# Kernel optimization log

Measured on AMD Instinct MI355X. Metric: run time of the kernel, lower is better.

## Reference

```python
import jax, jax.numpy as jnp
import numpy as np

L = 2          # num encoder layers
D = 256        # node_dim / d_model
H = 4          # nhead
FF = 4 * D     # dim_feedforward
GEO = 8        # geo feature dim (bi ++ bj)
HID = 512      # relation MLP hidden
C = 56         # num_rel_classes
N = 384        # number of nodes


def layer_norm(x, g, b, eps=1e-5):
    mu = jnp.mean(x, axis=-1, keepdims=True)
    var = jnp.mean((x - mu) ** 2, axis=-1, keepdims=True)
    return (x - mu) * jax.lax.rsqrt(var + eps) * g + b


def encoder_layer(x, wi, bi, wo, bo, w1, b1, w2, b2, g1, be1, g2, be2):
    # Post-norm torch TransformerEncoderLayer (norm_first=False, relu)
    n = x.shape[0]
    dh = D // H
    qkv = x @ wi + bi                                  # [n, 3D]
    q, k, v = jnp.split(qkv, 3, axis=-1)
    q = q.reshape(n, H, dh)
    k = k.reshape(n, H, dh)
    v = v.reshape(n, H, dh)
    scores = jnp.einsum('nhd,mhd->hnm', q, k) * (dh ** -0.5)
    attn = jax.nn.softmax(scores, axis=-1)
    o = jnp.einsum('hnm,mhd->nhd', attn, v).reshape(n, D) @ wo + bo
    x = layer_norm(x + o, g1, be1)
    f = jax.nn.relu(x @ w1 + b1) @ w2 + b2
    x = layer_norm(x + f, g2, be2)
    return x


def setup_inputs() -> dict:
    key = jax.random.key(0)
    ks = jax.random.split(key, 16)
    s = 0.02
    f32 = jnp.float32
    return {
        'node_feats': jax.random.normal(ks[0], (N, D), f32),
        'boxes_norm': jax.random.uniform(ks[1], (N, 4), dtype=f32),
        'attn_w_in': jax.random.normal(ks[2], (L, D, 3 * D), f32) * s,
        'attn_b_in': jnp.zeros((L, 3 * D), f32),
        'attn_w_out': jax.random.normal(ks[3], (L, D, D), f32) * s,
        'attn_b_out': jnp.zeros((L, D), f32),
        'ffn_w1': jax.random.normal(ks[4], (L, D, FF), f32) * s,
        'ffn_b1': jnp.zeros((L, FF), f32),
        'ffn_w2': jax.random.normal(ks[5], (L, FF, D), f32) * s,
        'ffn_b2': jnp.zeros((L, D), f32),
        'ln1_g': jnp.ones((L, D), f32),
        'ln1_b': jnp.zeros((L, D), f32),
        'ln2_g': jnp.ones((L, D), f32),
        'ln2_b': jnp.zeros((L, D), f32),
        'mlp_w1': jax.random.normal(ks[6], (2 * D + GEO, HID), f32) * s,
        'mlp_b1': jnp.zeros((HID,), f32),
        'mlp_w2': jax.random.normal(ks[7], (HID, C), f32) * s,
        'mlp_b2': jnp.zeros((C,), f32),
    }


def reference(node_feats, boxes_norm, attn_w_in, attn_b_in, attn_w_out,
              attn_b_out, ffn_w1, ffn_b1, ffn_w2, ffn_b2, ln1_g, ln1_b,
              ln2_g, ln2_b, mlp_w1, mlp_b1, mlp_w2, mlp_b2):
    x = node_feats
    for l in range(L):
        x = encoder_layer(x, attn_w_in[l], attn_b_in[l], attn_w_out[l],
                          attn_b_out[l], ffn_w1[l], ffn_b1[l], ffn_w2[l],
                          ffn_b2[l], ln1_g[l], ln1_b[l], ln2_g[l], ln2_b[l])
    n = node_feats.shape[0]
    # all ordered pairs (i, j), i != j, in row-major order matching the loop
    i_full = np.repeat(np.arange(n), n)
    j_full = np.tile(np.arange(n), n)
    keep = i_full != j_full
    idx_i = jnp.asarray(i_full[keep])
    idx_j = jnp.asarray(j_full[keep])
    rel_in = jnp.concatenate(
        [x[idx_i], x[idx_j], boxes_norm[idx_i], boxes_norm[idx_j]], axis=1)
    rel_logits = jax.nn.relu(rel_in @ mlp_w1 + mlp_b1) @ mlp_w2 + mlp_b2
    pair_idx = jnp.stack([idx_i, idx_j], axis=1)
    return (pair_idx, rel_logits)
```

## Files before the change

### kernel.cpp

```cpp
#include <hip/hip_runtime.h>

#define NN 384
#define DM 256
#define NH 4
#define FF 1024
#define HIDN 512
#define NCLS 56
#define NPAIR (NN*(NN-1))

typedef __attribute__((ext_vector_type(8))) short short8v;
typedef __attribute__((ext_vector_type(4))) float f32x4;
typedef __attribute__((ext_vector_type(16))) float f32x16;
typedef __attribute__((ext_vector_type(8))) unsigned short ushort8;
typedef __attribute__((ext_vector_type(4))) unsigned int uint4v;

static __device__ __forceinline__ unsigned short f2bf(float f) {
  unsigned u = __float_as_uint(f);
  unsigned r = u + 0x7fff + ((u >> 16) & 1);
  return (unsigned short)(r >> 16);
}
static __device__ __forceinline__ float bf2f(unsigned short v) {
  return __uint_as_float(((unsigned)v) << 16);
}
static __device__ __forceinline__ unsigned cvt_pk_bf16(float lo, float hi) {
  unsigned r;
  asm("v_cvt_pk_bf16_f32 %0, %1, %2" : "=v"(r) : "v"(lo), "v"(hi));
  return r;
}
#define MLROW(reg, half) (((reg) & 3) + 8 * ((reg) >> 2) + 4 * (half))

__global__ __launch_bounds__(256)
void pack_all(const float* __restrict__ wi, const float* __restrict__ wo,
              const float* __restrict__ w1, const float* __restrict__ w2,
              const float* __restrict__ mw1, const float* __restrict__ mw2,
              unsigned short* __restrict__ wi_f, unsigned short* __restrict__ wo_f,
              unsigned short* __restrict__ w1_f, unsigned short* __restrict__ w2_f,
              unsigned short* __restrict__ mw1_f, unsigned short* __restrict__ mw2_f) {
  int y = blockIdx.y, z = blockIdx.z;
  int t = blockIdx.x * 256 + threadIdx.x;
  const float* src; unsigned short* dst; int K, N; long sS, sD;
  switch (y) {
    case 0: src = wi;  dst = wi_f;  K = 256;  N = 768;  sS = 256L*768;  sD = 196608; break;
    case 1: src = wo;  dst = wo_f;  K = 256;  N = 256;  sS = 256L*256;  sD = 65536;  break;
    case 2: src = w1;  dst = w1_f;  K = 256;  N = 1024; sS = 256L*1024; sD = 262144; break;
    case 3: src = w2;  dst = w2_f;  K = 1024; N = 256;  sS = 1024L*256; sD = 262144; break;
    case 4: src = mw1; dst = mw1_f; K = 256;  N = 512;  sS = 256L*512;  sD = 131072; break;
    default: {
      if (z || t >= 4096) return;
      int l = t & 63, nt = (t >> 6) & 1, ks = t >> 7;
      int kb = ks * 16 + ((l >> 5) * 8), n = nt * 32 + (l & 31);
      #pragma unroll
      for (int r = 0; r < 8; ++r) {
        float v = (n < NCLS) ? mw2[(size_t)(kb + r) * NCLS + n] : 0.f;
        mw2_f[(size_t)t * 8 + r] = f2bf(v);
      }
      return;
    }
  }
  int Nt = N >> 5;
  int total = (K >> 4) * Nt * 64;
  if (t >= total) return;
  src += z * sS; dst += z * sD;
  int l = t & 63;
  int rem = t >> 6;
  int nt = rem % Nt, ks = rem / Nt;
  int kb = ks * 16 + ((l >> 5) * 8), n = nt * 32 + (l & 31);
  #pragma unroll
  for (int r = 0; r < 8; ++r)
    dst[(size_t)t * 8 + r] = f2bf(src[(size_t)(kb + r) * N + n]);
}

__global__ __launch_bounds__(256)
void x_init(const float* __restrict__ node, float* __restrict__ xbuf,
            unsigned short* __restrict__ xbf) {
  int i = blockIdx.x * 256 + threadIdx.x;
  float v = node[i];
  xbuf[i] = v;
  xbf[i] = f2bf(v);
}

__global__ __launch_bounds__(128)
void qkv_mfma(const unsigned short* __restrict__ xbf, const unsigned short* __restrict__ wif,
              const float* __restrict__ bi, unsigned short* __restrict__ qk,
              unsigned short* __restrict__ vt) {
  int id = blockIdx.x * 2 + (threadIdx.x >> 6);
  int lane = threadIdx.x & 63;
  int mt = id % 12, nt = id / 12;
  int col = lane & 31, half = lane >> 5;
  const unsigned short* asrc = xbf + (size_t)(mt * 32 + col) * 256 + half * 8;
  const unsigned short* bsrc = wif + ((size_t)nt * 64 + lane) * 8;
  f32x16 acc = {};
  #pragma unroll
  for (int ks = 0; ks < 16; ++ks) {
    short8v a = *reinterpret_cast<const short8v*>(asrc + ks * 16);
    short8v b = *reinterpret_cast<const short8v*>(bsrc + (size_t)ks * 24 * 512);
    acc = __builtin_amdgcn_mfma_f32_32x32x16_bf16(a, b, acc, 0, 0, 0);
  }
  int n = nt * 32 + col;
  float bb = bi[n];
  #pragma unroll
  for (int reg = 0; reg < 16; ++reg) {
    int row = mt * 32 + MLROW(reg, half);
    float v = acc[reg] + bb;
    if (n < 512) qk[(size_t)row * 512 + n] = f2bf(v);
    else         vt[(size_t)(n - 512) * 384 + row] = f2bf(v);
  }
}

__global__ __launch_bounds__(256)
void fused_attn(const unsigned short* __restrict__ qk, const unsigned short* __restrict__ vt,
                unsigned short* __restrict__ attno) {
  __shared__ float S[32][385];
  __shared__ unsigned short P[32][392];
  int n0 = blockIdx.x * 32;
  int h = blockIdx.y;
  int wave = threadIdx.x >> 6, lane = threadIdx.x & 63;
  int col = lane & 31, half = lane >> 5;
  {
    const unsigned short* asrc = qk + (size_t)(n0 + col) * 512 + h * 64 + half * 8;
    #pragma unroll
    for (int jj = 0; jj < 3; ++jj) {
      int ntk = wave * 3 + jj;
      const unsigned short* bsrc = qk + (size_t)(ntk * 32 + col) * 512 + 256 + h * 64 + half * 8;
      f32x16 acc = {};
      #pragma unroll
      for (int ks = 0; ks < 4; ++ks) {
        short8v a = *reinterpret_cast<const short8v*>(asrc + ks * 16);
        short8v b = *reinterpret_cast<const short8v*>(bsrc + ks * 16);
        acc = __builtin_amdgcn_mfma_f32_32x32x16_bf16(a, b, acc, 0, 0, 0);
      }
      #pragma unroll
      for (int reg = 0; reg < 16; ++reg)
        S[MLROW(reg, half)][ntk * 32 + col] = acc[reg] * 0.125f;
    }
  }
  __syncthreads();
  {
    int row = threadIdx.x >> 3, q = threadIdx.x & 7;
    float mx = -1e30f;
    #pragma unroll 8
    for (int c = 0; c < 48; ++c) mx = fmaxf(mx, S[row][q * 48 + c]);
    mx = fmaxf(mx, __shfl_xor(mx, 1));
    mx = fmaxf(mx, __shfl_xor(mx, 2));
    mx = fmaxf(mx, __shfl_xor(mx, 4));
    float sum = 0.f;
    #pragma unroll 8
    for (int c = 0; c < 48; ++c) {
      float e = __expf(S[row][q * 48 + c] - mx);
      S[row][q * 48 + c] = e;
      sum += e;
    }
    sum += __shfl_xor(sum, 1);
    sum += __shfl_xor(sum, 2);
    sum += __shfl_xor(sum, 4);
    float inv = 1.0f / sum;
    #pragma unroll 8
    for (int c = 0; c < 48; ++c)
      P[row][q * 48 + c] = f2bf(S[row][q * 48 + c] * inv);
  }
  __syncthreads();
  if (wave < 2) {
    int ntd = wave;
    const unsigned short* bsrc = vt + (size_t)(h * 64 + ntd * 32 + col) * 384 + half * 8;
    f32x16 acc = {};
    #pragma unroll
    for (int ks = 0; ks < 24; ++ks) {
      short8v a = *reinterpret_cast<const short8v*>(&P[col][ks * 16 + half * 8]);
      short8v b = *reinterpret_cast<const short8v*>(bsrc + ks * 16);
      acc = __builtin_amdgcn_mfma_f32_32x32x16_bf16(a, b, acc, 0, 0, 0);
    }
    #pragma unroll
    for (int reg = 0; reg < 16; ++reg)
      attno[(size_t)(n0 + MLROW(reg, half)) * 256 + h * 64 + ntd * 32 + col] =
          f2bf(acc[reg]);
  }
}

__global__ __launch_bounds__(256)
void add_ln(float* __restrict__ x, unsigned short* __restrict__ xbf,
            const float* __restrict__ r,
            const float* __restrict__ g, const float* __restrict__ b) {
  int i = blockIdx.x, t = threadIdx.x;
  float v = x[(size_t)i * DM + t] + r[(size_t)i * DM + t];
  __shared__ float red[256];
  red[t] = v; __syncthreads();
  for (int s = 128; s > 0; s >>= 1) { if (t < s) red[t] += red[t + s]; __syncthreads(); }
  float mu = red[0] * (1.0f / DM); __syncthreads();
  float dv = v - mu;
  red[t] = dv * dv; __syncthreads();
  for (int s = 128; s > 0; s >>= 1) { if (t < s) red[t] += red[t + s]; __syncthreads(); }
  float var = red[0] * (1.0f / DM);
  float inv = rsqrtf(var + 1e-5f);
  float o = dv * inv * g[t] + b[t];
  x[(size_t)i * DM + t] = o;
  xbf[(size_t)i * DM + t] = f2bf(o);
}

template<int OUT_BF16, int RELU, int NKS, int NT>
__global__ void mfma_gemm(const unsigned short* __restrict__ A, int lda, long sA,
               const unsigned short* __restrict__ Bfrag, long sB,
               const float* __restrict__ bias,
               float* __restrict__ Cf, unsigned short* __restrict__ Cb,
               int ldc, long sC, int Mt) {
  int id = blockIdx.x * (blockDim.x >> 6) + (threadIdx.x >> 6);
  if (id >= Mt * NT) return;
  int lane = threadIdx.x & 63;
  int mt = id % Mt, nt = id / Mt;
  int z = blockIdx.z;
  int col = lane & 31, half = lane >> 5;
  const unsigned short* asrc = A + z * sA + (size_t)(mt * 32 + col) * lda + half * 8;
  const unsigned short* bsrc = Bfrag + z * sB + ((size_t)nt * 64 + lane) * 8;
  f32x16 acc = {};
  #pragma unroll
  for (int ks = 0; ks < NKS; ++ks) {
    short8v a = *reinterpret_cast<const short8v*>(asrc + ks * 16);
    short8v b = *reinterpret_cast<const short8v*>(bsrc + (size_t)ks * NT * 512);
    acc = __builtin_amdgcn_mfma_f32_32x32x16_bf16(a, b, acc, 0, 0, 0);
  }
  int n = nt * 32 + col;
  float bb = bias ? bias[n] : 0.f;
  #pragma unroll
  for (int reg = 0; reg < 16; ++reg) {
    int row = mt * 32 + MLROW(reg, half);
    float v = acc[reg] + bb;
    if (RELU) v = fmaxf(v, 0.f);
    if (OUT_BF16) Cb[z * sC + (size_t)row * ldc + n] = f2bf(v);
    else          Cf[z * sC + (size_t)row * ldc + n] = v;
  }
}

__global__ __launch_bounds__(128)
void uv_gemm(const unsigned short* __restrict__ xbf, const unsigned short* __restrict__ mw1f,
             const float* __restrict__ mw1, const float* __restrict__ b1,
             const float* __restrict__ boxes,
             float* __restrict__ U, unsigned short* __restrict__ Vbf) {
  int id = blockIdx.x * 2 + (threadIdx.x >> 6);
  int lane = threadIdx.x & 63;
  int z = blockIdx.z;
  int mt = id % 12, nt = id / 12;
  int col = lane & 31, half = lane >> 5;
  const unsigned short* asrc = xbf + (size_t)(mt * 32 + col) * 256 + half * 8;
  const unsigned short* bsrc = mw1f + (size_t)z * 131072 + ((size_t)nt * 64 + lane) * 8;
  f32x16 acc = {};
  #pragma unroll
  for (int ks = 0; ks < 16; ++ks) {
    short8v a = *reinterpret_cast<const short8v*>(asrc + ks * 16);
    short8v b = *reinterpret_cast<const short8v*>(bsrc + (size_t)ks * 16 * 512);
    acc = __builtin_amdgcn_mfma_f32_32x32x16_bf16(a, b, acc, 0, 0, 0);
  }
  int n = nt * 32 + col;
  float w0 = mw1[(size_t)(512 + z * 4 + 0) * HIDN + n];
  float w1r = mw1[(size_t)(512 + z * 4 + 1) * HIDN + n];
  float w2r = mw1[(size_t)(512 + z * 4 + 2) * HIDN + n];
  float w3 = mw1[(size_t)(512 + z * 4 + 3) * HIDN + n];
  float bb = (z == 0) ? b1[n] : 0.f;
  #pragma unroll
  for (int reg = 0; reg < 16; ++reg) {
    int row = mt * 32 + MLROW(reg, half);
    const float* bx = boxes + row * 4;
    float v = acc[reg] + bb + bx[0] * w0 + bx[1] * w1r + bx[2] * w2r + bx[3] * w3;
    if (z == 0) U[(size_t)row * HIDN + n] = v;
    else        Vbf[(size_t)row * HIDN + n] = f2bf(v);
  }
}

__global__ __launch_bounds__(256)
void pair_idx_kernel(float* __restrict__ out) {
  int p = blockIdx.x * 256 + threadIdx.x;
  if (p >= NPAIR) return;
  int i = p / (NN - 1);
  int r = p - i * (NN - 1);
  int j = r + (r >= i ? 1 : 0);
  out[2 * p + 0] = (float)i;
  out[2 * p + 1] = (float)j;
}

__global__ __launch_bounds__(512, 2)
void pair_mfma(const float* __restrict__ U, const unsigned short* __restrict__ Vbf,
               const unsigned short* __restrict__ w2frag,
               const float* __restrict__ b2, float* __restrict__ out) {
  __shared__ unsigned short w2l[32768];
  #pragma unroll
  for (int p = 0; p < 8; ++p) {
    int off = p * 4096 + threadIdx.x * 8;
    *reinterpret_cast<uint4v*>(&w2l[off]) =
        *reinterpret_cast<const uint4v*>(w2frag + off);
  }
  __syncthreads();

  int wave = threadIdx.x >> 6, lane = threadIdx.x & 63;
  int task = blockIdx.x * 8 + wave;
  int ip = task / 12, jt = task % 12;
  int i0 = ip * 2;
  int col = lane & 31, half = lane >> 5;
  int j_row = jt * 32 + col;

  const unsigned short* vsrc = Vbf + (size_t)j_row * HIDN + half * 8;
  const float* u0 = U + (size_t)i0 * HIDN + half * 8;
  const float* u1 = u0 + HIDN;
  const unsigned short* bsrc = w2l + (size_t)lane * 8;

  f32x16 acc00 = {}, acc01 = {}, acc10 = {}, acc11 = {};
  #pragma unroll
  for (int ks = 0; ks < 32; ++ks) {
    ushort8 v8 = *reinterpret_cast<const ushort8*>(vsrc + ks * 16);
    short8v b0 = *reinterpret_cast<const short8v*>(bsrc + (size_t)(ks * 2 + 0) * 512);
    short8v b1v = *reinterpret_cast<const short8v*>(bsrc + (size_t)(ks * 2 + 1) * 512);
    float4 ua0 = *reinterpret_cast<const float4*>(u0 + ks * 16);
    float4 ub0 = *reinterpret_cast<const float4*>(u0 + ks * 16 + 4);
    float4 ua1 = *reinterpret_cast<const float4*>(u1 + ks * 16);
    float4 ub1 = *reinterpret_cast<const float4*>(u1 + ks * 16 + 4);
    float v0 = bf2f(v8[0]), v1 = bf2f(v8[1]), v2 = bf2f(v8[2]), v3 = bf2f(v8[3]);
    float v4 = bf2f(v8[4]), v5 = bf2f(v8[5]), v6 = bf2f(v8[6]), v7 = bf2f(v8[7]);
    uint4v pk0;
    pk0[0] = cvt_pk_bf16(fmaxf(v0 + ua0.x, 0.f), fmaxf(v1 + ua0.y, 0.f));
    pk0[1] = cvt_pk_bf16(fmaxf(v2 + ua0.z, 0.f), fmaxf(v3 + ua0.w, 0.f));
    pk0[2] = cvt_pk_bf16(fmaxf(v4 + ub0.x, 0.f), fmaxf(v5 + ub0.y, 0.f));
    pk0[3] = cvt_pk_bf16(fmaxf(v6 + ub0.z, 0.f), fmaxf(v7 + ub0.w, 0.f));
    short8v a0 = *reinterpret_cast<short8v*>(&pk0);
    acc00 = __builtin_amdgcn_mfma_f32_32x32x16_bf16(a0, b0, acc00, 0, 0, 0);
    acc01 = __builtin_amdgcn_mfma_f32_32x32x16_bf16(a0, b1v, acc01, 0, 0, 0);
    uint4v pk1;
    pk1[0] = cvt_pk_bf16(fmaxf(v0 + ua1.x, 0.f), fmaxf(v1 + ua1.y, 0.f));
    pk1[1] = cvt_pk_bf16(fmaxf(v2 + ua1.z, 0.f), fmaxf(v3 + ua1.w, 0.f));
    pk1[2] = cvt_pk_bf16(fmaxf(v4 + ub1.x, 0.f), fmaxf(v5 + ub1.y, 0.f));
    pk1[3] = cvt_pk_bf16(fmaxf(v6 + ub1.z, 0.f), fmaxf(v7 + ub1.w, 0.f));
    short8v a1 = *reinterpret_cast<short8v*>(&pk1);
    acc10 = __builtin_amdgcn_mfma_f32_32x32x16_bf16(a1, b0, acc10, 0, 0, 0);
    acc11 = __builtin_amdgcn_mfma_f32_32x32x16_bf16(a1, b1v, acc11, 0, 0, 0);
  }

  float b2v0 = b2[col];
  float b2v1 = (32 + col < NCLS) ? b2[32 + col] : 0.f;
  float* lg = out + 2 * (size_t)NPAIR;
  int i1 = i0 + 1;
  #pragma unroll
  for (int reg = 0; reg < 16; ++reg) {
    int j = jt * 32 + MLROW(reg, half);
    if (j != i0) {
      int p = i0 * (NN - 1) + (j > i0 ? j - 1 : j);
      float* row = lg + (size_t)p * NCLS;
      row[col] = acc00[reg] + b2v0;
      if (col < NCLS - 32) row[32 + col] = acc01[reg] + b2v1;
    }
    if (j != i1) {
      int p = i1 * (NN - 1) + (j > i1 ? j - 1 : j);
      float* row = lg + (size_t)p * NCLS;
      row[col] = acc10[reg] + b2v0;
      if (col < NCLS - 32) row[32 + col] = acc11[reg] + b2v1;
    }
  }
}

extern "C" void kernel_launch(void* const* d_in, const int* in_sizes, int n_in,
                              void* d_out, int out_size, void* d_ws, size_t ws_size,
                              hipStream_t stream) {
  const float* node   = (const float*)d_in[0];
  const float* boxes  = (const float*)d_in[1];
  const float* w_in   = (const float*)d_in[2];
  const float* b_in   = (const float*)d_in[3];
  const float* w_out  = (const float*)d_in[4];
  const float* b_out  = (const float*)d_in[5];
  const float* fw1    = (const float*)d_in[6];
  const float* fb1    = (const float*)d_in[7];
  const float* fw2    = (const float*)d_in[8];
  const float* fb2    = (const float*)d_in[9];
  const float* ln1g   = (const float*)d_in[10];
  const float* ln1b   = (const float*)d_in[11];
  const float* ln2g   = (const float*)d_in[12];
  const float* ln2b   = (const float*)d_in[13];
  const float* mw1    = (const float*)d_in[14];
  const float* mb1    = (const float*)d_in[15];
  const float* mw2    = (const float*)d_in[16];
  const float* mb2    = (const float*)d_in[17];
  float* out = (float*)d_out;

  float* ws = (float*)d_ws;
  float* xbuf = ws;
  float* proj = xbuf + 98304;
  float* U    = proj + 98304;
  unsigned short* us = (unsigned short*)(U + 196608);
  unsigned short* x_bf   = us;             us += 98304;
  unsigned short* qk_bf  = us;             us += 196608;
  unsigned short* vt_bf  = us;             us += 98304;
  unsigned short* at_bf  = us;             us += 98304;
  unsigned short* ffh_bf = us;             us += 393216;
  unsigned short* Vbf    = us;             us += 196608;
  unsigned short* wi_f   = us;             us += 393216;
  unsigned short* wo_f   = us;             us += 131072;
  unsigned short* fw1_f  = us;             us += 524288;
  unsigned short* fw2_f  = us;             us += 524288;
  unsigned short* mw1_f  = us;             us += 262144;
  unsigned short* w2_f   = us;             us += 32768;

  pack_all<<<dim3(128, 6, 2), 256, 0, stream>>>(w_in, w_out, fw1, fw2, mw1, mw2,
                                                wi_f, wo_f, fw1_f, fw2_f, mw1_f, w2_f);
  pair_idx_kernel<<<dim3((NPAIR + 255) / 256), 256, 0, stream>>>(out);
  x_init<<<dim3(384), 256, 0, stream>>>(node, xbuf, x_bf);

  for (int l = 0; l < 2; ++l) {
    qkv_mfma<<<dim3(144), 128, 0, stream>>>(x_bf, wi_f + (size_t)l * 196608,
                                            b_in + (size_t)l * 768, qk_bf, vt_bf);
    fused_attn<<<dim3(12, 4), 256, 0, stream>>>(qk_bf, vt_bf, at_bf);
    mfma_gemm<0, 0, 16, 8><<<dim3(48), 128, 0, stream>>>(
        at_bf, 256, 0, wo_f + (size_t)l * 65536, 0, b_out + (size_t)l * 256,
        proj, nullptr, 256, 0, 12);
    add_ln<<<dim3(NN), 256, 0, stream>>>(xbuf, x_bf, proj,
                                         ln1g + (size_t)l * 256, ln1b + (size_t)l * 256);
    mfma_gemm<1, 1, 16, 32><<<dim3(192), 128, 0, stream>>>(
        x_bf, 256, 0, fw1_f + (size_t)l * 262144, 0, fb1 + (size_t)l * 1024,
        nullptr, ffh_bf, 1024, 0, 12);
    mfma_gemm<0, 0, 64, 8><<<dim3(48), 128, 0, stream>>>(
        ffh_bf, 1024, 0, fw2_f + (size_t)l * 262144, 0, fb2 + (size_t)l * 256,
        proj, nullptr, 256, 0, 12);
    add_ln<<<dim3(NN), 256, 0, stream>>>(xbuf, x_bf, proj,
                                         ln2g + (size_t)l * 256, ln2b + (size_t)l * 256);
  }

  uv_gemm<<<dim3(96, 1, 2), 128, 0, stream>>>(x_bf, mw1_f, mw1, mb1, boxes, U, Vbf);
  pair_mfma<<<dim3(288), 512, 0, stream>>>(U, Vbf, w2_f, mb2, out);
}
```

Before: 136.9 us.

## Fuse encoder stages into one persistent kernel with global barriers

Replaces the chain of roughly twenty small kernel launches (weight packing, init, QKV, attention, projections, layernorms, FFN, UV GEMM) with a single persistent 48-block kernel that separates stages with atomic-counter grid barriers. Layernorm is rewritten to use one wave per row with shuffle reductions and single-pass mean and variance. The aim is to remove launch overhead and tail gaps between the many tiny stages. In exchange, only 48 blocks run, so each stage has far less parallelism than its own launch had. The spin barrier also depends on all 48 blocks being resident at once, and the counter is cleared by a memset every call.

```diff
diff --git a/kernel.cpp b/kernel.cpp
--- a/kernel.cpp
+++ b/kernel.cpp
@@ -7,6 +7,7 @@
 #define HIDN 512
 #define NCLS 56
 #define NPAIR (NN*(NN-1))
+#define NBLK 48
 
 typedef __attribute__((ext_vector_type(8))) short short8v;
 typedef __attribute__((ext_vector_type(4))) float f32x4;
@@ -29,187 +30,21 @@
 }
 #define MLROW(reg, half) (((reg) & 3) + 8 * ((reg) >> 2) + 4 * (half))
 
-__global__ __launch_bounds__(256)
-void pack_all(const float* __restrict__ wi, const float* __restrict__ wo,
-              const float* __restrict__ w1, const float* __restrict__ w2,
-              const float* __restrict__ mw1, const float* __restrict__ mw2,
-              unsigned short* __restrict__ wi_f, unsigned short* __restrict__ wo_f,
-              unsigned short* __restrict__ w1_f, unsigned short* __restrict__ w2_f,
-              unsigned short* __restrict__ mw1_f, unsigned short* __restrict__ mw2_f) {
-  int y = blockIdx.y, z = blockIdx.z;
-  int t = blockIdx.x * 256 + threadIdx.x;
-  const float* src; unsigned short* dst; int K, N; long sS, sD;
-  switch (y) {
-    case 0: src = wi;  dst = wi_f;  K = 256;  N = 768;  sS = 256L*768;  sD = 196608; break;
-    case 1: src = wo;  dst = wo_f;  K = 256;  N = 256;  sS = 256L*256;  sD = 65536;  break;
-    case 2: src = w1;  dst = w1_f;  K = 256;  N = 1024; sS = 256L*1024; sD = 262144; break;
-    case 3: src = w2;  dst = w2_f;  K = 1024; N = 256;  sS = 1024L*256; sD = 262144; break;
-    case 4: src = mw1; dst = mw1_f; K = 256;  N = 512;  sS = 256L*512;  sD = 131072; break;
-    default: {
-      if (z || t >= 4096) return;
-      int l = t & 63, nt = (t >> 6) & 1, ks = t >> 7;
-      int kb = ks * 16 + ((l >> 5) * 8), n = nt * 32 + (l & 31);
-      #pragma unroll
-      for (int r = 0; r < 8; ++r) {
-        float v = (n < NCLS) ? mw2[(size_t)(kb + r) * NCLS + n] : 0.f;
-        mw2_f[(size_t)t * 8 + r] = f2bf(v);
-      }
-      return;
-    }
-  }
-  int Nt = N >> 5;
-  int total = (K >> 4) * Nt * 64;
-  if (t >= total) return;
-  src += z * sS; dst += z * sD;
-  int l = t & 63;
-  int rem = t >> 6;
-  int nt = rem % Nt, ks = rem / Nt;
-  int kb = ks * 16 + ((l >> 5) * 8), n = nt * 32 + (l & 31);
-  #pragma unroll
-  for (int r = 0; r < 8; ++r)
-    dst[(size_t)t * 8 + r] = f2bf(src[(size_t)(kb + r) * N + n]);
-}
-
-__global__ __launch_bounds__(256)
-void x_init(const float* __restrict__ node, float* __restrict__ xbuf,
-            unsigned short* __restrict__ xbf) {
-  int i = blockIdx.x * 256 + threadIdx.x;
-  float v = node[i];
-  xbuf[i] = v;
-  xbf[i] = f2bf(v);
-}
-
-__global__ __launch_bounds__(128)
-void qkv_mfma(const unsigned short* __restrict__ xbf, const unsigned short* __restrict__ wif,
-              const float* __restrict__ bi, unsigned short* __restrict__ qk,
-              unsigned short* __restrict__ vt) {
-  int id = blockIdx.x * 2 + (threadIdx.x >> 6);
-  int lane = threadIdx.x & 63;
-  int mt = id % 12, nt = id / 12;
-  int col = lane & 31, half = lane >> 5;
-  const unsigned short* asrc = xbf + (size_t)(mt * 32 + col) * 256 + half * 8;
-  const unsigned short* bsrc = wif + ((size_t)nt * 64 + lane) * 8;
-  f32x16 acc = {};
-  #pragma unroll
-  for (int ks = 0; ks < 16; ++ks) {
-    short8v a = *reinterpret_cast<const short8v*>(asrc + ks * 16);
-    short8v b = *reinterpret_cast<const short8v*>(bsrc + (size_t)ks * 24 * 512);
-    acc = __builtin_amdgcn_mfma_f32_32x32x16_bf16(a, b, acc, 0, 0, 0);
-  }
-  int n = nt * 32 + col;
-  float bb = bi[n];
-  #pragma unroll
-  for (int reg = 0; reg < 16; ++reg) {
-    int row = mt * 32 + MLROW(reg, half);
-    float v = acc[reg] + bb;
-    if (n < 512) qk[(size_t)row * 512 + n] = f2bf(v);
-    else         vt[(size_t)(n - 512) * 384 + row] = f2bf(v);
-  }
-}
-
-__global__ __launch_bounds__(256)
-void fused_attn(const unsigned short* __restrict__ qk, const unsigned short* __restrict__ vt,
-                unsigned short* __restrict__ attno) {
-  __shared__ float S[32][385];
-  __shared__ unsigned short P[32][392];
-  int n0 = blockIdx.x * 32;
-  int h = blockIdx.y;
-  int wave = threadIdx.x >> 6, lane = threadIdx.x & 63;
-  int col = lane & 31, half = lane >> 5;
-  {
-    const unsigned short* asrc = qk + (size_t)(n0 + col) * 512 + h * 64 + half * 8;
-    #pragma unroll
-    for (int jj = 0; jj < 3; ++jj) {
-      int ntk = wave * 3 + jj;
-      const unsigned short* bsrc = qk + (size_t)(ntk * 32 + col) * 512 + 256 + h * 64 + half * 8;
-      f32x16 acc = {};
-      #pragma unroll
-      for (int ks = 0; ks < 4; ++ks) {
-        short8v a = *reinterpret_cast<const short8v*>(asrc + ks * 16);
-        short8v b = *reinterpret_cast<const short8v*>(bsrc + ks * 16);
-        acc = __builtin_amdgcn_mfma_f32_32x32x16_bf16(a, b, acc, 0, 0, 0);
-      }
-      #pragma unroll
-      for (int reg = 0; reg < 16; ++reg)
-        S[MLROW(reg, half)][ntk * 32 + col] = acc[reg] * 0.125f;
-    }
-  }
+static __device__ __forceinline__ void gsync(unsigned* bar, int ph) {
   __syncthreads();
-  {
-    int row = threadIdx.x >> 3, q = threadIdx.x & 7;
-    float mx = -1e30f;
-    #pragma unroll 8
-    for (int c = 0; c < 48; ++c) mx = fmaxf(mx, S[row][q * 48 + c]);
-    mx = fmaxf(mx, __shfl_xor(mx, 1));
-    mx = fmaxf(mx, __shfl_xor(mx, 2));
-    mx = fmaxf(mx, __shfl_xor(mx, 4));
-    float sum = 0.f;
-    #pragma unroll 8
-    for (int c = 0; c < 48; ++c) {
-      float e = __expf(S[row][q * 48 + c] - mx);
-      S[row][q * 48 + c] = e;
-      sum += e;
-    }
-    sum += __shfl_xor(sum, 1);
-    sum += __shfl_xor(sum, 2);
-    sum += __shfl_xor(sum, 4);
-    float inv = 1.0f / sum;
-    #pragma unroll 8
-    for (int c = 0; c < 48; ++c)
-      P[row][q * 48 + c] = f2bf(S[row][q * 48 + c] * inv);
+  if (threadIdx.x == 0) {
+    __threadfence();
+    atomicAdd(bar + ph, 1u);
+    while (atomicAdd(bar + ph, 0u) < (unsigned)NBLK)
+      __builtin_amdgcn_s_sleep(1);
   }
   __syncthreads();
-  if (wave < 2) {
-    int ntd = wave;
-    const unsigned short* bsrc = vt + (size_t)(h * 64 + ntd * 32 + col) * 384 + half * 8;
-    f32x16 acc = {};
-    #pragma unroll
-    for (int ks = 0; ks < 24; ++ks) {
-      short8v a = *reinterpret_cast<const short8v*>(&P[col][ks * 16 + half * 8]);
-      short8v b = *reinterpret_cast<const short8v*>(bsrc + ks * 16);
-      acc = __builtin_amdgcn_mfma_f32_32x32x16_bf16(a, b, acc, 0, 0, 0);
-    }
-    #pragma unroll
-    for (int reg = 0; reg < 16; ++reg)
-      attno[(size_t)(n0 + MLROW(reg, half)) * 256 + h * 64 + ntd * 32 + col] =
-          f2bf(acc[reg]);
-  }
-}
-
-__global__ __launch_bounds__(256)
-void add_ln(float* __restrict__ x, unsigned short* __restrict__ xbf,
-            const float* __restrict__ r,
-            const float* __restrict__ g, const float* __restrict__ b) {
-  int i = blockIdx.x, t = threadIdx.x;
-  float v = x[(size_t)i * DM + t] + r[(size_t)i * DM + t];
-  __shared__ float red[256];
-  red[t] = v; __syncthreads();
-  for (int s = 128; s > 0; s >>= 1) { if (t < s) red[t] += red[t + s]; __syncthreads(); }
-  float mu = red[0] * (1.0f / DM); __syncthreads();
-  float dv = v - mu;
-  red[t] = dv * dv; __syncthreads();
-  for (int s = 128; s > 0; s >>= 1) { if (t < s) red[t] += red[t + s]; __syncthreads(); }
-  float var = red[0] * (1.0f / DM);
-  float inv = rsqrtf(var + 1e-5f);
-  float o = dv * inv * g[t] + b[t];
-  x[(size_t)i * DM + t] = o;
-  xbf[(size_t)i * DM + t] = f2bf(o);
-}
-
-template<int OUT_BF16, int RELU, int NKS, int NT>
-__global__ void mfma_gemm(const unsigned short* __restrict__ A, int lda, long sA,
-               const unsigned short* __restrict__ Bfrag, long sB,
-               const float* __restrict__ bias,
-               float* __restrict__ Cf, unsigned short* __restrict__ Cb,
-               int ldc, long sC, int Mt) {
-  int id = blockIdx.x * (blockDim.x >> 6) + (threadIdx.x >> 6);
-  if (id >= Mt * NT) return;
-  int lane = threadIdx.x & 63;
-  int mt = id % Mt, nt = id / Mt;
-  int z = blockIdx.z;
-  int col = lane & 31, half = lane >> 5;
-  const unsigned short* asrc = A + z * sA + (size_t)(mt * 32 + col) * lda + half * 8;
-  const unsigned short* bsrc = Bfrag + z * sB + ((size_t)nt * 64 + lane) * 8;
+  __threadfence();
+}
+
+template<int NKS, int NT>
+static __device__ __forceinline__ f32x16 mfma_tile(const unsigned short* __restrict__ asrc,
+                                                   const unsigned short* __restrict__ bsrc) {
   f32x16 acc = {};
   #pragma unroll
   for (int ks = 0; ks < NKS; ++ks) {
@@ -217,62 +52,299 @@
     short8v b = *reinterpret_cast<const short8v*>(bsrc + (size_t)ks * NT * 512);
     acc = __builtin_amdgcn_mfma_f32_32x32x16_bf16(a, b, acc, 0, 0, 0);
   }
-  int n = nt * 32 + col;
-  float bb = bias ? bias[n] : 0.f;
-  #pragma unroll
-  for (int reg = 0; reg < 16; ++reg) {
-    int row = mt * 32 + MLROW(reg, half);
-    float v = acc[reg] + bb;
-    if (RELU) v = fmaxf(v, 0.f);
-    if (OUT_BF16) Cb[z * sC + (size_t)row * ldc + n] = f2bf(v);
-    else          Cf[z * sC + (size_t)row * ldc + n] = v;
-  }
-}
-
-__global__ __launch_bounds__(128)
-void uv_gemm(const unsigned short* __restrict__ xbf, const unsigned short* __restrict__ mw1f,
-             const float* __restrict__ mw1, const float* __restrict__ b1,
-             const float* __restrict__ boxes,
-             float* __restrict__ U, unsigned short* __restrict__ Vbf) {
-  int id = blockIdx.x * 2 + (threadIdx.x >> 6);
-  int lane = threadIdx.x & 63;
-  int z = blockIdx.z;
-  int mt = id % 12, nt = id / 12;
+  return acc;
+}
+
+__global__ __launch_bounds__(256)
+void fused_enc(const float* __restrict__ node, const float* __restrict__ boxes,
+               const float* __restrict__ w_in, const float* __restrict__ b_in,
+               const float* __restrict__ w_out, const float* __restrict__ b_out,
+               const float* __restrict__ fw1, const float* __restrict__ fb1,
+               const float* __restrict__ fw2, const float* __restrict__ fb2,
+               const float* __restrict__ ln1g, const float* __restrict__ ln1b,
+               const float* __restrict__ ln2g, const float* __restrict__ ln2b,
+               const float* __restrict__ mw1, const float* __restrict__ mb1,
+               const float* __restrict__ mw2,
+               float* __restrict__ xbuf, float* __restrict__ proj, float* __restrict__ U,
+               unsigned short* __restrict__ x_bf, unsigned short* __restrict__ qk_bf,
+               unsigned short* __restrict__ vt_bf, unsigned short* __restrict__ at_bf,
+               unsigned short* __restrict__ ffh_bf, unsigned short* __restrict__ Vbf,
+               unsigned short* __restrict__ wi_f, unsigned short* __restrict__ wo_f,
+               unsigned short* __restrict__ fw1_f, unsigned short* __restrict__ fw2_f,
+               unsigned short* __restrict__ mw1_f, unsigned short* __restrict__ w2_f,
+               float* __restrict__ out, unsigned* __restrict__ bar) {
+  __shared__ float S[32][385];
+  __shared__ unsigned short P[32][392];
+  int tid = threadIdx.x;
+  int wave = tid >> 6, lane = tid & 63;
+  int wid = blockIdx.x * 4 + wave;
   int col = lane & 31, half = lane >> 5;
-  const unsigned short* asrc = xbf + (size_t)(mt * 32 + col) * 256 + half * 8;
-  const unsigned short* bsrc = mw1f + (size_t)z * 131072 + ((size_t)nt * 64 + lane) * 8;
-  f32x16 acc = {};
-  #pragma unroll
-  for (int ks = 0; ks < 16; ++ks) {
-    short8v a = *reinterpret_cast<const short8v*>(asrc + ks * 16);
-    short8v b = *reinterpret_cast<const short8v*>(bsrc + (size_t)ks * 16 * 512);
-    acc = __builtin_amdgcn_mfma_f32_32x32x16_bf16(a, b, acc, 0, 0, 0);
-  }
-  int n = nt * 32 + col;
-  float w0 = mw1[(size_t)(512 + z * 4 + 0) * HIDN + n];
-  float w1r = mw1[(size_t)(512 + z * 4 + 1) * HIDN + n];
-  float w2r = mw1[(size_t)(512 + z * 4 + 2) * HIDN + n];
-  float w3 = mw1[(size_t)(512 + z * 4 + 3) * HIDN + n];
-  float bb = (z == 0) ? b1[n] : 0.f;
-  #pragma unroll
-  for (int reg = 0; reg < 16; ++reg) {
-    int row = mt * 32 + MLROW(reg, half);
-    const float* bx = boxes + row * 4;
-    float v = acc[reg] + bb + bx[0] * w0 + bx[1] * w1r + bx[2] * w2r + bx[3] * w3;
-    if (z == 0) U[(size_t)row * HIDN + n] = v;
-    else        Vbf[(size_t)row * HIDN + n] = f2bf(v);
-  }
-}
-
-__global__ __launch_bounds__(256)
-void pair_idx_kernel(float* __restrict__ out) {
-  int p = blockIdx.x * 256 + threadIdx.x;
-  if (p >= NPAIR) return;
-  int i = p / (NN - 1);
-  int r = p - i * (NN - 1);
-  int j = r + (r >= i ? 1 : 0);
-  out[2 * p + 0] = (float)i;
-  out[2 * p + 1] = (float)j;
+  int gtid = blockIdx.x * 256 + tid;
+  int ph = 0;
+
+  for (int t0 = gtid; t0 < 233472; t0 += NBLK * 256) {
+    int tt = t0; const float* src; unsigned short* dst; int N;
+    if (tt < 49152)       { int z = tt / 24576; tt -= z * 24576; src = w_in  + (size_t)z * 196608; dst = wi_f  + (size_t)z * 196608; N = 768; }
+    else if (tt < 65536)  { tt -= 49152;  int z = tt / 8192;  tt -= z * 8192;  src = w_out + (size_t)z * 65536;  dst = wo_f  + (size_t)z * 65536;  N = 256; }
+    else if (tt < 131072) { tt -= 65536;  int z = tt / 32768; tt -= z * 32768; src = fw1   + (size_t)z * 262144; dst = fw1_f + (size_t)z * 262144; N = 1024; }
+    else if (tt < 196608) { tt -= 131072; int z = tt / 32768; tt -= z * 32768; src = fw2   + (size_t)z * 262144; dst = fw2_f + (size_t)z * 262144; N = 256; }
+    else if (tt < 229376) { tt -= 196608; int z = tt / 16384; tt -= z * 16384; src = mw1   + (size_t)z * 131072; dst = mw1_f + (size_t)z * 131072; N = 512; }
+    else                  { tt -= 229376; src = mw2; dst = w2_f; N = 0; }
+    int l = tt & 63, rem = tt >> 6;
+    if (N) {
+      int Nt = N >> 5;
+      int nt = rem % Nt, ks = rem / Nt;
+      int kb = ks * 16 + ((l >> 5) * 8), n = nt * 32 + (l & 31);
+      #pragma unroll
+      for (int r = 0; r < 8; ++r)
+        dst[(size_t)tt * 8 + r] = f2bf(src[(size_t)(kb + r) * N + n]);
+    } else {
+      int nt = rem & 1, ks = rem >> 1;
+      int kb = ks * 16 + ((l >> 5) * 8), n = nt * 32 + (l & 31);
+      #pragma unroll
+      for (int r = 0; r < 8; ++r) {
+        float v = (n < NCLS) ? mw2[(size_t)(kb + r) * NCLS + n] : 0.f;
+        dst[(size_t)tt * 8 + r] = f2bf(v);
+      }
+    }
+  }
+  for (int t = gtid; t < 24576; t += NBLK * 256) {
+    float4 v = reinterpret_cast<const float4*>(node)[t];
+    reinterpret_cast<float4*>(xbuf)[t] = v;
+    uint2 pk;
+    pk.x = cvt_pk_bf16(v.x, v.y);
+    pk.y = cvt_pk_bf16(v.z, v.w);
+    *reinterpret_cast<uint2*>(x_bf + (size_t)t * 4) = pk;
+  }
+  for (int t = gtid; t < NPAIR; t += NBLK * 256) {
+    int i = t / (NN - 1);
+    int r = t - i * (NN - 1);
+    int j = r + (r >= i ? 1 : 0);
+    out[2 * t + 0] = (float)i;
+    out[2 * t + 1] = (float)j;
+  }
+  gsync(bar, ph++);
+
+  for (int l = 0; l < 2; ++l) {
+    const unsigned short* wi_fl  = wi_f  + (size_t)l * 196608;
+    const unsigned short* wo_fl  = wo_f  + (size_t)l * 65536;
+    const unsigned short* fw1_fl = fw1_f + (size_t)l * 262144;
+    const unsigned short* fw2_fl = fw2_f + (size_t)l * 262144;
+    const float* bi = b_in + (size_t)l * 768;
+    const float* bo = b_out + (size_t)l * 256;
+    const float* b1l = fb1 + (size_t)l * 1024;
+    const float* b2l = fb2 + (size_t)l * 256;
+
+    for (int t = wid; t < 288; t += 192) {
+      int mt = t % 12, nt = t / 12;
+      const unsigned short* asrc = x_bf + (size_t)(mt * 32 + col) * 256 + half * 8;
+      const unsigned short* bsrc = wi_fl + ((size_t)nt * 64 + lane) * 8;
+      f32x16 acc = mfma_tile<16, 24>(asrc, bsrc);
+      int n = nt * 32 + col;
+      float bb = bi[n];
+      #pragma unroll
+      for (int reg = 0; reg < 16; ++reg) {
+        int row = mt * 32 + MLROW(reg, half);
+        float v = acc[reg] + bb;
+        if (n < 512) qk_bf[(size_t)row * 512 + n] = f2bf(v);
+        else         vt_bf[(size_t)(n - 512) * 384 + row] = f2bf(v);
+      }
+    }
+    gsync(bar, ph++);
+
+    {
+      int n0 = (blockIdx.x % 12) * 32;
+      int h = blockIdx.x / 12;
+      {
+        const unsigned short* asrc = qk_bf + (size_t)(n0 + col) * 512 + h * 64 + half * 8;
+        #pragma unroll
+        for (int jj = 0; jj < 3; ++jj) {
+          int ntk = wave * 3 + jj;
+          const unsigned short* bsrc = qk_bf + (size_t)(ntk * 32 + col) * 512 + 256 + h * 64 + half * 8;
+          f32x16 acc = {};
+          #pragma unroll
+          for (int ks = 0; ks < 4; ++ks) {
+            short8v a = *reinterpret_cast<const short8v*>(asrc + ks * 16);
+            short8v b = *reinterpret_cast<const short8v*>(bsrc + ks * 16);
+            acc = __builtin_amdgcn_mfma_f32_32x32x16_bf16(a, b, acc, 0, 0, 0);
+          }
+          #pragma unroll
+          for (int reg = 0; reg < 16; ++reg)
+            S[MLROW(reg, half)][ntk * 32 + col] = acc[reg] * 0.125f;
+        }
+      }
+      __syncthreads();
+      {
+        int row = tid >> 3, q = tid & 7;
+        float mx = -1e30f;
+        #pragma unroll 8
+        for (int c = 0; c < 48; ++c) mx = fmaxf(mx, S[row][q * 48 + c]);
+        mx = fmaxf(mx, __shfl_xor(mx, 1));
+        mx = fmaxf(mx, __shfl_xor(mx, 2));
+        mx = fmaxf(mx, __shfl_xor(mx, 4));
+        float sum = 0.f;
+        #pragma unroll 8
+        for (int c = 0; c < 48; ++c) {
+          float e = __expf(S[row][q * 48 + c] - mx);
+          S[row][q * 48 + c] = e;
+          sum += e;
+        }
+        sum += __shfl_xor(sum, 1);
+        sum += __shfl_xor(sum, 2);
+        sum += __shfl_xor(sum, 4);
+        float inv = 1.0f / sum;
+        #pragma unroll 8
+        for (int c = 0; c < 48; ++c)
+          P[row][q * 48 + c] = f2bf(S[row][q * 48 + c] * inv);
+      }
+      __syncthreads();
+      if (wave < 2) {
+        int ntd = wave;
+        const unsigned short* bsrc = vt_bf + (size_t)(h * 64 + ntd * 32 + col) * 384 + half * 8;
+        f32x16 acc = {};
+        #pragma unroll
+        for (int ks = 0; ks < 24; ++ks) {
+          short8v a = *reinterpret_cast<const short8v*>(&P[col][ks * 16 + half * 8]);
+          short8v b = *reinterpret_cast<const short8v*>(bsrc + ks * 16);
+          acc = __builtin_amdgcn_mfma_f32_32x32x16_bf16(a, b, acc, 0, 0, 0);
+        }
+        #pragma unroll
+        for (int reg = 0; reg < 16; ++reg)
+          at_bf[(size_t)(n0 + MLROW(reg, half)) * 256 + h * 64 + ntd * 32 + col] =
+              f2bf(acc[reg]);
+      }
+    }
+    gsync(bar, ph++);
+
+    for (int t = wid; t < 96; t += 192) {
+      int mt = t % 12, nt = t / 12;
+      const unsigned short* asrc = at_bf + (size_t)(mt * 32 + col) * 256 + half * 8;
+      const unsigned short* bsrc = wo_fl + ((size_t)nt * 64 + lane) * 8;
+      f32x16 acc = mfma_tile<16, 8>(asrc, bsrc);
+      int n = nt * 32 + col;
+      float bb = bo[n];
+      #pragma unroll
+      for (int reg = 0; reg < 16; ++reg)
+        proj[(size_t)(mt * 32 + MLROW(reg, half)) * 256 + n] = acc[reg] + bb;
+    }
+    gsync(bar, ph++);
+
+    {
+      const float* g = ln1g + (size_t)l * 256;
+      const float* be = ln1b + (size_t)l * 256;
+      for (int row = wid; row < 384; row += 192) {
+        float4 pr = reinterpret_cast<const float4*>(proj + (size_t)row * 256)[lane];
+        float4 xr = reinterpret_cast<const float4*>(xbuf + (size_t)row * 256)[lane];
+        float v0 = pr.x + xr.x, v1 = pr.y + xr.y, v2 = pr.z + xr.z, v3 = pr.w + xr.w;
+        float s = v0 + v1 + v2 + v3;
+        float s2 = v0 * v0 + v1 * v1 + v2 * v2 + v3 * v3;
+        #pragma unroll
+        for (int off = 1; off < 64; off <<= 1) {
+          s += __shfl_xor(s, off);
+          s2 += __shfl_xor(s2, off);
+        }
+        float mu = s * (1.0f / 256.0f);
+        float var = s2 * (1.0f / 256.0f) - mu * mu;
+        float inv = rsqrtf(var + 1e-5f);
+        float4 g4 = reinterpret_cast<const float4*>(g)[lane];
+        float4 b4 = reinterpret_cast<const float4*>(be)[lane];
+        float o0 = (v0 - mu) * inv * g4.x + b4.x;
+        float o1 = (v1 - mu) * inv * g4.y + b4.y;
+        float o2 = (v2 - mu) * inv * g4.z + b4.z;
+        float o3 = (v3 - mu) * inv * g4.w + b4.w;
+        float4 o4 = make_float4(o0, o1, o2, o3);
+        reinterpret_cast<float4*>(xbuf + (size_t)row * 256)[lane] = o4;
+        uint2 pk;
+        pk.x = cvt_pk_bf16(o0, o1);
+        pk.y = cvt_pk_bf16(o2, o3);
+        *reinterpret_cast<uint2*>(x_bf + (size_t)row * 256 + lane * 4) = pk;
+      }
+    }
+    gsync(bar, ph++);
+
+    for (int t = wid; t < 384; t += 192) {
+      int mt = t % 12, nt = t / 12;
+      const unsigned short* asrc = x_bf + (size_t)(mt * 32 + col) * 256 + half * 8;
+      const unsigned short* bsrc = fw1_fl + ((size_t)nt * 64 + lane) * 8;
+      f32x16 acc = mfma_tile<16, 32>(asrc, bsrc);
+      int n = nt * 32 + col;
+      float bb = b1l[n];
+      #pragma unroll
+      for (int reg = 0; reg < 16; ++reg) {
+        int row = mt * 32 + MLROW(reg, half);
+        ffh_bf[(size_t)row * 1024 + n] = f2bf(fmaxf(acc[reg] + bb, 0.f));
+      }
+    }
+    gsync(bar, ph++);
+
+    for (int t = wid; t < 96; t += 192) {
+      int mt = t % 12, nt = t / 12;
+      const unsigned short* asrc = ffh_bf + (size_t)(mt * 32 + col) * 1024 + half * 8;
+      const unsigned short* bsrc = fw2_fl + ((size_t)nt * 64 + lane) * 8;
+      f32x16 acc = mfma_tile<64, 8>(asrc, bsrc);
+      int n = nt * 32 + col;
+      float bb = b2l[n];
+      #pragma unroll
+      for (int reg = 0; reg < 16; ++reg)
+        proj[(size_t)(mt * 32 + MLROW(reg, half)) * 256 + n] = acc[reg] + bb;
+    }
+    gsync(bar, ph++);
+
+    {
+      const float* g = ln2g + (size_t)l * 256;
+      const float* be = ln2b + (size_t)l * 256;
+      for (int row = wid; row < 384; row += 192) {
+        float4 pr = reinterpret_cast<const float4*>(proj + (size_t)row * 256)[lane];
+        float4 xr = reinterpret_cast<const float4*>(xbuf + (size_t)row * 256)[lane];
+        float v0 = pr.x + xr.x, v1 = pr.y + xr.y, v2 = pr.z + xr.z, v3 = pr.w + xr.w;
+        float s = v0 + v1 + v2 + v3;
+        float s2 = v0 * v0 + v1 * v1 + v2 * v2 + v3 * v3;
+        #pragma unroll
+        for (int off = 1; off < 64; off <<= 1) {
+          s += __shfl_xor(s, off);
+          s2 += __shfl_xor(s2, off);
+        }
+        float mu = s * (1.0f / 256.0f);
+        float var = s2 * (1.0f / 256.0f) - mu * mu;
+        float inv = rsqrtf(var + 1e-5f);
+        float4 g4 = reinterpret_cast<const float4*>(g)[lane];
+        float4 b4 = reinterpret_cast<const float4*>(be)[lane];
+        float o0 = (v0 - mu) * inv * g4.x + b4.x;
+        float o1 = (v1 - mu) * inv * g4.y + b4.y;
+        float o2 = (v2 - mu) * inv * g4.z + b4.z;
+        float o3 = (v3 - mu) * inv * g4.w + b4.w;
+        float4 o4 = make_float4(o0, o1, o2, o3);
+        reinterpret_cast<float4*>(xbuf + (size_t)row * 256)[lane] = o4;
+        uint2 pk;
+        pk.x = cvt_pk_bf16(o0, o1);
+        pk.y = cvt_pk_bf16(o2, o3);
+        *reinterpret_cast<uint2*>(x_bf + (size_t)row * 256 + lane * 4) = pk;
+      }
+    }
+    gsync(bar, ph++);
+  }
+
+  for (int t = wid; t < 384; t += 192) {
+    int z = t / 192, id = t % 192;
+    int mt = id % 12, nt = id / 12;
+    const unsigned short* asrc = x_bf + (size_t)(mt * 32 + col) * 256 + half * 8;
+    const unsigned short* bsrc = mw1_f + (size_t)z * 131072 + ((size_t)nt * 64 + lane) * 8;
+    f32x16 acc = mfma_tile<16, 16>(asrc, bsrc);
+    int n = nt * 32 + col;
+    float w0 = mw1[(size_t)(512 + z * 4 + 0) * HIDN + n];
+    float w1r = mw1[(size_t)(512 + z * 4 + 1) * HIDN + n];
+    float w2r = mw1[(size_t)(512 + z * 4 + 2) * HIDN + n];
+    float w3 = mw1[(size_t)(512 + z * 4 + 3) * HIDN + n];
+    float bb = (z == 0) ? mb1[n] : 0.f;
+    #pragma unroll
+    for (int reg = 0; reg < 16; ++reg) {
+      int row = mt * 32 + MLROW(reg, half);
+      const float* bx = boxes + row * 4;
+      float v = acc[reg] + bb + bx[0] * w0 + bx[1] * w1r + bx[2] * w2r + bx[3] * w3;
+      if (z == 0) U[(size_t)row * HIDN + n] = v;
+      else        Vbf[(size_t)row * HIDN + n] = f2bf(v);
+    }
+  }
 }
 
 __global__ __launch_bounds__(512, 2)
@@ -392,31 +464,13 @@
   unsigned short* fw2_f  = us;             us += 524288;
   unsigned short* mw1_f  = us;             us += 262144;
   unsigned short* w2_f   = us;             us += 32768;
-
-  pack_all<<<dim3(128, 6, 2), 256, 0, stream>>>(w_in, w_out, fw1, fw2, mw1, mw2,
-                                                wi_f, wo_f, fw1_f, fw2_f, mw1_f, w2_f);
-  pair_idx_kernel<<<dim3((NPAIR + 255) / 256), 256, 0, stream>>>(out);
-  x_init<<<dim3(384), 256, 0, stream>>>(node, xbuf, x_bf);
-
-  for (int l = 0; l < 2; ++l) {
-    qkv_mfma<<<dim3(144), 128, 0, stream>>>(x_bf, wi_f + (size_t)l * 196608,
-                                            b_in + (size_t)l * 768, qk_bf, vt_bf);
-    fused_attn<<<dim3(12, 4), 256, 0, stream>>>(qk_bf, vt_bf, at_bf);
-    mfma_gemm<0, 0, 16, 8><<<dim3(48), 128, 0, stream>>>(
-        at_bf, 256, 0, wo_f + (size_t)l * 65536, 0, b_out + (size_t)l * 256,
-        proj, nullptr, 256, 0, 12);
-    add_ln<<<dim3(NN), 256, 0, stream>>>(xbuf, x_bf, proj,
-                                         ln1g + (size_t)l * 256, ln1b + (size_t)l * 256);
-    mfma_gemm<1, 1, 16, 32><<<dim3(192), 128, 0, stream>>>(
-        x_bf, 256, 0, fw1_f + (size_t)l * 262144, 0, fb1 + (size_t)l * 1024,
-        nullptr, ffh_bf, 1024, 0, 12);
-    mfma_gemm<0, 0, 64, 8><<<dim3(48), 128, 0, stream>>>(
-        ffh_bf, 1024, 0, fw2_f + (size_t)l * 262144, 0, fb2 + (size_t)l * 256,
-        proj, nullptr, 256, 0, 12);
-    add_ln<<<dim3(NN), 256, 0, stream>>>(xbuf, x_bf, proj,
-                                         ln2g + (size_t)l * 256, ln2b + (size_t)l * 256);
-  }
-
-  uv_gemm<<<dim3(96, 1, 2), 128, 0, stream>>>(x_bf, mw1_f, mw1, mb1, boxes, U, Vbf);
-  pair_mfma<<<dim3(288), 512, 0, stream>>>(U, Vbf, w2_f, mb2, out);
-}
+  unsigned* bar = (unsigned*)us;
+
+  hipMemsetAsync(bar, 0, 64, stream);
+  fused_enc<<<dim3(NBLK), dim3(256), 0, stream>>>(
+      node, boxes, w_in, b_in, w_out, b_out, fw1, fb1, fw2, fb2,
+      ln1g, ln1b, ln2g, ln2b, mw1, mb1, mw2,
+      xbuf, proj, U, x_bf, qk_bf, vt_bf, at_bf, ffh_bf, Vbf,
+      wi_f, wo_f, fw1_f, fw2_f, mw1_f, w2_f, out, bar);
+  pair_mfma<<<dim3(288), dim3(512), 0, stream>>>(U, Vbf, w2_f, mb2, out);
+}
```

Result: slower. 260.4 us (+90.2%).
